# Optimization experiments

Measured on AMD Instinct MI355X. Metric: run time of the kernel, lower is better.

## Reference

```python
import jax, jax.numpy as jnp
import numpy as np

TAU = 0.02        # System2Reasoner softmax temperature
TOP_K = 50        # retrieval top-k
ALPHA = 1.0       # visual/text prototype mixing
TAU_CONF = 0.8    # entropy confidence threshold


def _normalize(x):
    return x / jnp.maximum(jnp.linalg.norm(x, axis=-1, keepdims=True), 1e-12)


def _entropy(logits):
    p = jax.nn.softmax(logits, axis=-1)
    return -jnp.sum(p * jnp.log(p + 1e-10))


def setup_inputs() -> dict:
    key = jax.random.key(0)
    k1, k2, k3, k4, k5, k6 = jax.random.split(key, 6)
    D, P, M, C = 768, 2048, 65536, 1000
    test_global = _normalize(jax.random.normal(k1, (1, D), dtype=jnp.float32))
    test_patches = _normalize(jax.random.normal(k2, (P, D), dtype=jnp.float32))
    memory_nodes = _normalize(jax.random.normal(k3, (M, D), dtype=jnp.float32))
    textual_anchors = _normalize(jax.random.normal(k4, (C, D), dtype=jnp.float32))
    class_sums = jax.random.normal(k5, (C, D), dtype=jnp.float32)
    class_counts = jax.random.uniform(k6, (C,), dtype=jnp.float32) * 100.0 + 1.0
    return {
        "test_global": test_global,
        "test_patches": test_patches,
        "memory_nodes": memory_nodes,
        "textual_anchors": textual_anchors,
        "class_sums": class_sums,
        "class_counts": class_counts,
        "max_steps": 3,
    }


def reference(test_global, test_patches, memory_nodes, textual_anchors,
              class_sums, class_counts, max_steps):
    # System-1 prototypes
    safe_counts = jnp.maximum(class_counts, 1.0)[:, None]            # [C,1]
    visual_protos = _normalize(class_sums / safe_counts)             # [C,D]
    protos = _normalize(textual_anchors + ALPHA * visual_protos)     # [C,D]

    sys1_logits = 100.0 * test_global @ protos.T                     # [1,C]
    active0 = _entropy(sys1_logits) > TAU_CONF

    def body(carry, _):
        patches, logits, step, active = carry
        # message passing: topk cosine-sim retrieval + softmax-weighted gather
        sim = patches @ memory_nodes.T                               # [P,M]
        topv, topi = jax.lax.top_k(sim, TOP_K)                       # [P,K]
        attn = jax.nn.softmax(topv / TAU, axis=1)                    # [P,K]
        gathered = memory_nodes[topi]                                # [P,K,D]
        messages = jnp.einsum('pk,pkd->pd', attn, gathered)          # [P,D]
        new_patches = _normalize(patches + messages)
        # token evidence pooling
        ev = jnp.max(new_patches @ textual_anchors.T, axis=-1, keepdims=True)  # [P,1]
        w = jax.nn.softmax(ev / TAU, axis=0)                         # [P,1]
        g = _normalize(jnp.sum(new_patches * w, axis=0, keepdims=True))        # [1,D]
        new_logits = 100.0 * g @ protos.T                            # [1,C]
        # only commit updates while the entropy loop is still active
        patches = jnp.where(active, new_patches, patches)
        logits = jnp.where(active, new_logits, logits)
        step = step + active.astype(jnp.int32)
        active = jnp.logical_and(active, _entropy(new_logits) > TAU_CONF)
        return (patches, logits, step, active), None

    (patches, final_logits, step, _), _ = jax.lax.scan(
        body, (test_patches, sys1_logits, jnp.int32(0), active0),
        None, length=max_steps)
    return final_logits, step
```

## Files before the change

### kernel.cpp

```cpp
#include <hip/hip_runtime.h>
#include <hip/hip_bf16.h>
#include <stdint.h>


typedef __attribute__((ext_vector_type(8))) short short8;
typedef __attribute__((ext_vector_type(4))) float f32x4;
typedef __attribute__((ext_vector_type(4))) int   i32x4;

#define DIM    768
#define NPATCH 2048
#define NMEM   65536
#define NCLS   1000
#define NSAMP  4096
#define CAP    1024
#define PRESEL 64
#define PCAP   128
#define TAUINV 50.0f

__device__ __forceinline__ unsigned short f2bf(float f){
  unsigned b = __float_as_uint(f);
  b += 0x7FFFu + ((b >> 16) & 1u);
  return (unsigned short)(b >> 16);
}
__device__ __forceinline__ unsigned encf(float x){
  unsigned b = __float_as_uint(x);
  return (b & 0x80000000u) ? ~b : (b | 0x80000000u);
}
__device__ __forceinline__ float decf(unsigned k){
  unsigned b = (k & 0x80000000u) ? (k & 0x7FFFFFFFu) : ~k;
  return __uint_as_float(b);
}
__device__ __forceinline__ void gload16(const void* g, void* l){
  __builtin_amdgcn_global_load_lds(
      (const __attribute__((address_space(1))) unsigned int*)g,
      (__attribute__((address_space(3))) unsigned int*)l, 16, 0, 0);
}
__device__ __forceinline__ uint4 pack8(float4 a, float4 b){
  uint4 u;
  u.x = (unsigned)f2bf(a.x) | ((unsigned)f2bf(a.y) << 16);
  u.y = (unsigned)f2bf(a.z) | ((unsigned)f2bf(a.w) << 16);
  u.z = (unsigned)f2bf(b.x) | ((unsigned)f2bf(b.y) << 16);
  u.w = (unsigned)f2bf(b.z) | ((unsigned)f2bf(b.w) << 16);
  return u;
}
__device__ __forceinline__ uint4 packq16(const float* s, float inv){
  unsigned wd[4];
  #pragma unroll
  for (int k = 0; k < 4; ++k){
    unsigned v = 0;
    #pragma unroll
    for (int j = 0; j < 4; ++j){
      int q = __float2int_rn(s[k*4 + j] * inv);
      q = q > 127 ? 127 : (q < -127 ? -127 : q);
      v |= ((unsigned)(q & 255)) << (8*j);
    }
    wd[k] = v;
  }
  return make_uint4(wd[0], wd[1], wd[2], wd[3]);
}

__device__ __forceinline__ unsigned select_kth(const unsigned* keys, int n, int k,
                                               unsigned* hist, int t)
{
  __syncthreads();
  if (t == 0){ hist[256] = 0u; hist[257] = (unsigned)k; }
  __syncthreads();
  for (int pass = 0; pass < 4; ++pass){
    int shift = 24 - 8*pass;
    hist[t] = 0u;
    __syncthreads();
    unsigned pref = hist[256];
    for (int i = t; i < n; i += 256){
      unsigned key = keys[i];
      bool ok = (pass == 0) || ((key >> (shift + 8)) == pref);
      if (ok) atomicAdd(&hist[(key >> shift) & 255u], 1u);
    }
    __syncthreads();
    if (t == 0){
      unsigned krem = hist[257];
      unsigned cum = 0u; int b = 255;
      for (; b >= 0; --b){ cum += hist[b]; if (cum >= krem) break; }
      if (b < 0) b = 0;
      unsigned above = cum - hist[b];
      hist[257] = krem - above;
      hist[256] = (pref << 8) | (unsigned)b;
    }
    __syncthreads();
  }
  return hist[256];
}

__global__ __launch_bounds__(256) void proto_kernel(
    const float* __restrict__ anchors, const float* __restrict__ sums,
    const float* __restrict__ counts, float* __restrict__ protos,
    unsigned short* __restrict__ anchors_bf)
{
  int c = blockIdx.x, t = threadIdx.x;
  if (c >= NCLS){
    for (int j = 0; j < 3; ++j) anchors_bf[(size_t)c*DIM + t + j*256] = 0;
    return;
  }
  __shared__ float wv[4]; __shared__ float bc;
  float cnt = fmaxf(counts[c], 1.0f);
  float v[3];
  #pragma unroll
  for (int j = 0; j < 3; ++j) v[j] = sums[(size_t)c*DIM + t + j*256] / cnt;
  float ss = v[0]*v[0] + v[1]*v[1] + v[2]*v[2];
  for (int off = 32; off > 0; off >>= 1) ss += __shfl_down(ss, off, 64);
  if ((t & 63) == 0) wv[t >> 6] = ss;
  __syncthreads();
  if (t == 0) bc = wv[0] + wv[1] + wv[2] + wv[3];
  __syncthreads();
  float rn = 1.0f / fmaxf(sqrtf(bc), 1e-12f);
  __syncthreads();
  float pr[3];
  #pragma unroll
  for (int j = 0; j < 3; ++j){
    int d = t + j*256;
    float a = anchors[(size_t)c*DIM + d];
    pr[j] = a + v[j] * rn;
    int dd = (d & ~63) | ((((d >> 3) ^ c) & 7) << 3) | (d & 7);
    anchors_bf[(size_t)c*DIM + dd] = f2bf(a);
  }
  ss = pr[0]*pr[0] + pr[1]*pr[1] + pr[2]*pr[2];
  for (int off = 32; off > 0; off >>= 1) ss += __shfl_down(ss, off, 64);
  if ((t & 63) == 0) wv[t >> 6] = ss;
  __syncthreads();
  if (t == 0) bc = wv[0] + wv[1] + wv[2] + wv[3];
  __syncthreads();
  float rn2 = 1.0f / fmaxf(sqrtf(bc), 1e-12f);
  #pragma unroll
  for (int j = 0; j < 3; ++j) protos[(size_t)c*DIM + t + j*256] = pr[j] * rn2;
}

__global__ __launch_bounds__(256) void prep_patches(
    const float* __restrict__ tp, float* __restrict__ pc)
{
  size_t i = (size_t)blockIdx.x*256 + threadIdx.x;
  *(float4*)(pc + i*4) = *(const float4*)(tp + i*4);
}

__global__ __launch_bounds__(512) void conv_i8_kernel(
    const float* __restrict__ src, signed char* __restrict__ dst,
    float* __restrict__ scales)
{
  int w = threadIdx.x >> 6, lane = threadIdx.x & 63;
  int row = blockIdx.x*8 + w;
  const float* r = src + (size_t)row*DIM;
  float x[16]; float mx = 0.f;
  if (lane < 48){
    #pragma unroll
    for (int j = 0; j < 4; ++j){
      float4 v = *(const float4*)(r + lane*16 + j*4);
      x[j*4+0] = v.x; x[j*4+1] = v.y; x[j*4+2] = v.z; x[j*4+3] = v.w;
      mx = fmaxf(mx, fmaxf(fmaxf(fabsf(v.x), fabsf(v.y)), fmaxf(fabsf(v.z), fabsf(v.w))));
    }
  }
  for (int off = 32; off > 0; off >>= 1) mx = fmaxf(mx, __shfl_xor(mx, off, 64));
  if (lane == 0) scales[row] = mx / 127.0f;
  float inv = (mx > 0.f) ? 127.0f / mx : 0.f;
  if (lane < 48){
    int ks = lane >> 2, c = lane & 3;
    uint4 u = packq16(x, inv);
    *(uint4*)(dst + (size_t)row*DIM + ks*64 + ((c ^ ((row >> 1) & 3))*16)) = u;
  }
}

__global__ __launch_bounds__(256) void slab_init(
    const float* __restrict__ pc, unsigned short* __restrict__ slab,
    signed char* __restrict__ sli8, float* __restrict__ spb)
{
  __shared__ __align__(16) float gl[DIM];
  __shared__ float wv[4]; __shared__ float bc;
  int p = blockIdx.x, t = threadIdx.x;
  float a0 = pc[(size_t)p*DIM + t], a1 = pc[(size_t)p*DIM + t + 256],
        a2 = pc[(size_t)p*DIM + t + 512];
  gl[t] = a0; gl[t + 256] = a1; gl[t + 512] = a2;
  float am = fmaxf(fabsf(a0), fmaxf(fabsf(a1), fabsf(a2)));
  for (int off = 32; off > 0; off >>= 1) am = fmaxf(am, __shfl_down(am, off, 64));
  if ((t & 63) == 0) wv[t >> 6] = am;
  __syncthreads();
  if (t == 0) bc = fmaxf(fmaxf(wv[0], wv[1]), fmaxf(wv[2], wv[3]));
  __syncthreads();
  float mx = bc;
  float inv8 = (mx > 0.f) ? 127.0f / mx : 0.f;
  if (t < 96){
    int ks2 = t >> 3, c8 = t & 7;
    const float* sblk = &gl[ks2*64 + c8*8];
    uint4 u = pack8(*(const float4*)sblk, *(const float4*)(sblk + 4));
    *(uint4*)((char*)slab + (((size_t)ks2*NPATCH + p)*128) + ((size_t)(c8 ^ (p & 7))*16)) = u;
  }
  if (t < 48){
    int ks2 = t >> 2, c = t & 3;
    uint4 u = packq16(&gl[t*16], inv8);
    *(uint4*)(sli8 + ((size_t)ks2*NPATCH + p)*64 + ((c ^ ((p >> 1) & 3))*16)) = u;
  }
  if (t == 0) spb[p] = mx / 127.0f;
}

template<int MODE, int NT>
__global__ __launch_bounds__(256, 3) void gemm8_kernel(
    const signed char* __restrict__ Ai8, const float* __restrict__ sA, int rowbase,
    const signed char* __restrict__ Bslab, const float* __restrict__ sB,
    const float* __restrict__ thresholds,
    int* __restrict__ counters,
    int* __restrict__ cand_idx,
    float* __restrict__ cand_score,
    float* __restrict__ sims_sample,
    const int* __restrict__ active)
{
  if (*active == 0) return;
  __shared__ __align__(16) signed char Al[128*64];
  __shared__ __align__(16) signed char Bl[128*64];
  int b = blockIdx.x, nwg = gridDim.x;
  int wg = (b & 7)*(nwg >> 3) + (b >> 3);
  int mt0 = (wg >> 4) * NT, pt = wg & 15;
  int t = threadIdx.x, w = t >> 6, lane = t & 63, l15 = lane & 15, l4 = lane >> 4;
  int wr = w >> 1, wc = w & 1;
  int pbase = pt*128;

  float thv[4], sbv[4];
  #pragma unroll
  for (int g = 0; g < 4; ++g){
    int patch = pbase + wc*64 + g*16 + l15;
    if (MODE == 0) thv[g] = thresholds[patch];
    sbv[g] = sB[patch];
  }

  i32x4 acc[4][4];
  #pragma unroll
  for (int x = 0; x < 4; ++x)
    #pragma unroll
    for (int y = 0; y < 4; ++y) acc[x][y] = (i32x4){0, 0, 0, 0};

  const int NSTEP = NT * 12;
  for (int s = 0; s < NSTEP; ++s){
    int tile = s / 12, ks = s % 12;
    if (s) __syncthreads();
    size_t arow0 = (size_t)rowbase + ((size_t)(mt0 + tile))*128;
    #pragma unroll
    for (int i = 0; i < 2; ++i){
      int g = w*64 + i*256 + lane;
      const void* ga = Ai8 + (arow0 + (g >> 2))*(size_t)DIM + ks*64 + (g & 3)*16;
      gload16(ga, (char*)Al + (w*64 + i*256)*16);
      const void* gb = Bslab + ((size_t)ks*NPATCH + pbase)*64 + (size_t)g*16;
      gload16(gb, (char*)Bl + (w*64 + i*256)*16);
    }
    __syncthreads();

    i32x4 af[4], bfr[4];
    #pragma unroll
    for (int ng = 0; ng < 4; ++ng){
      int row = wr*64 + ng*16 + l15;
      af[ng] = *(const i32x4*)(Al + row*64 + ((l4 ^ ((row >> 1) & 3))*16));
    }
    #pragma unroll
    for (int g = 0; g < 4; ++g){
      int row = wc*64 + g*16 + l15;
      bfr[g] = *(const i32x4*)(Bl + row*64 + ((l4 ^ ((row >> 1) & 3))*16));
    }
    #pragma unroll
    for (int ng = 0; ng < 4; ++ng)
      #pragma unroll
      for (int g = 0; g < 4; ++g)
        acc[ng][g] = __builtin_amdgcn_mfma_i32_16x16x64_i8(af[ng], bfr[g], acc[ng][g], 0, 0, 0);

    if (ks == 11){
      int nodebase = rowbase + (mt0 + tile)*128 + wr*64;
      if (MODE == 0){
        #pragma unroll
        for (int g = 0; g < 4; ++g){
          int patch = pbase + wc*64 + g*16 + l15;
          float th = thv[g], sb = sbv[g];
          #pragma unroll
          for (int ng = 0; ng < 4; ++ng){
            f32x4 sa = *(const f32x4*)(sA + nodebase + ng*16 + l4*4);
            #pragma unroll
            for (int i = 0; i < 4; ++i){
              float v = (float)acc[ng][g][i] * sa[i] * sb;
              if (v >= th){
                int node = nodebase + ng*16 + l4*4 + i;
                int pos = atomicAdd(&counters[patch], 1);
                if (pos < CAP){
                  cand_idx[(size_t)patch*CAP + pos]   = node;
                  cand_score[(size_t)patch*CAP + pos] = v;
                }
              }
            }
          }
        }
      } else {
        #pragma unroll
        for (int g = 0; g < 4; ++g){
          int patch = pbase + wc*64 + g*16 + l15;
          float sb = sbv[g];
          #pragma unroll
          for (int ng = 0; ng < 4; ++ng){
            f32x4 sa = *(const f32x4*)(sA + nodebase + ng*16 + l4*4);
            f32x4 v;
            #pragma unroll
            for (int i = 0; i < 4; ++i) v[i] = (float)acc[ng][g][i] * sa[i] * sb;
            int col = nodebase + ng*16 + l4*4;
            *(f32x4*)(sims_sample + (size_t)patch*NSAMP + col) = v;
          }
        }
      }
      if (tile + 1 < NT){
        #pragma unroll
        for (int x = 0; x < 4; ++x)
          #pragma unroll
          for (int y = 0; y < 4; ++y) acc[x][y] = (i32x4){0, 0, 0, 0};
      }
    }
  }
}

__global__ __launch_bounds__(256, 3) void gemm_ev_kernel(
    const unsigned short* __restrict__ Abf,
    const unsigned short* __restrict__ Bslab,
    unsigned* __restrict__ ev_key,
    const int* __restrict__ active)
{
  if (*active == 0) return;
  __shared__ __align__(16) unsigned short Al[128*64];
  __shared__ __align__(16) unsigned short Bl[128*64];
  int b = blockIdx.x, nwg = gridDim.x;
  int wg = (b & 7)*(nwg >> 3) + (b >> 3);
  int mt = wg >> 4, pt = wg & 15;
  int t = threadIdx.x, w = t >> 6, lane = t & 63, l15 = lane & 15, l4 = lane >> 4;
  int wr = w >> 1, wc = w & 1;
  int pbase = pt*128;
  int srow = w*8 + (lane >> 3);
  int scol = (lane & 7)*16;
  const char* Ab = (const char*)Abf;
  const char* Bb = (const char*)Bslab;

  f32x4 acc[4][4];
  #pragma unroll
  for (int x = 0; x < 4; ++x)
    #pragma unroll
    for (int y = 0; y < 4; ++y) acc[x][y] = (f32x4){0.f, 0.f, 0.f, 0.f};

  for (int s = 0; s < 12; ++s){
    if (s) __syncthreads();
    size_t arow0 = (size_t)mt*128;
    #pragma unroll
    for (int i = 0; i < 4; ++i){
      const void* ga = Ab + ((arow0 + srow + i*32)*(size_t)(DIM*2)) + s*128 + scol;
      gload16(ga, (char*)Al + i*4096 + w*1024);
      const void* gb = Bb + (((size_t)s*NPATCH + pbase)*128) + i*4096 + w*1024 + lane*16;
      gload16(gb, (char*)Bl + i*4096 + w*1024);
    }
    __syncthreads();
    short8 af[2][4], bf_[2][4];
    #pragma unroll
    for (int kk = 0; kk < 2; ++kk){
      #pragma unroll
      for (int ng = 0; ng < 4; ++ng){
        int row = wr*64 + ng*16 + l15;
        int slot = (kk*4 + l4) ^ (row & 7);
        af[kk][ng] = *(const short8*)((const char*)Al + row*128 + slot*16);
      }
      #pragma unroll
      for (int g = 0; g < 4; ++g){
        int row = wc*64 + g*16 + l15;
        int slot = (kk*4 + l4) ^ (row & 7);
        bf_[kk][g] = *(const short8*)((const char*)Bl + row*128 + slot*16);
      }
    }
    #pragma unroll
    for (int kk = 0; kk < 2; ++kk)
      #pragma unroll
      for (int ng = 0; ng < 4; ++ng)
        #pragma unroll
        for (int g = 0; g < 4; ++g)
          acc[ng][g] = __builtin_amdgcn_mfma_f32_16x16x32_bf16(af[kk][ng], bf_[kk][g], acc[ng][g], 0, 0, 0);
  }

  #pragma unroll
  for (int g = 0; g < 4; ++g){
    int patch = pbase + wc*64 + g*16 + l15;
    float m = -3e38f; bool any = false;
    #pragma unroll
    for (int ng = 0; ng < 4; ++ng){
      #pragma unroll
      for (int i = 0; i < 4; ++i){
        int a = mt*128 + wr*64 + ng*16 + l4*4 + i;
        if (a < NCLS){ m = fmaxf(m, acc[ng][g][i]); any = true; }
      }
    }
    if (any) atomicMax(&ev_key[patch], encf(m));
  }
}

__global__ __launch_bounds__(256) void thresh_kernel(
    const float* __restrict__ sims, float* __restrict__ thresholds,
    int* __restrict__ counters, int* __restrict__ cand_idx,
    float* __restrict__ cand_score, unsigned* __restrict__ ev_key,
    const int* __restrict__ active)
{
  if (*active == 0) return;
  __shared__ unsigned keys[NSAMP];
  __shared__ unsigned hist[258];
  __shared__ int lcnt;
  int p = blockIdx.x, t = threadIdx.x;
  const float4* src = (const float4*)(sims + (size_t)p*NSAMP);
  for (int i = t; i < NSAMP/4; i += 256){
    float4 v = src[i];
    keys[i*4+0] = encf(v.x); keys[i*4+1] = encf(v.y);
    keys[i*4+2] = encf(v.z); keys[i*4+3] = encf(v.w);
  }
  unsigned kth = select_kth(keys, NSAMP, 16, hist, t);
  if (t == 0){ thresholds[p] = decf(kth); ev_key[p] = 0u; lcnt = 0; }
  __syncthreads();
  for (int i = t; i < NSAMP; i += 256){
    unsigned key = keys[i];
    if (key >= kth){
      int pos = atomicAdd(&lcnt, 1);
      if (pos < CAP){
        cand_idx[(size_t)p*CAP + pos]   = i;
        cand_score[(size_t)p*CAP + pos] = decf(key);
      }
    }
  }
  __syncthreads();
  if (t == 0) counters[p] = lcnt < CAP ? lcnt : CAP;
}

__global__ __launch_bounds__(256) void msg_kernel(
    const int* __restrict__ counters, const int* __restrict__ cand_idx,
    const float* __restrict__ cand_score, const float* __restrict__ memf,
    float* __restrict__ pc, unsigned short* __restrict__ slab,
    signed char* __restrict__ sli8, float* __restrict__ spb,
    const int* __restrict__ active)
{
  if (*active == 0) return;
  __shared__ unsigned sk[CAP]; __shared__ int si[CAP];
  __shared__ __align__(16) float gl[DIM];
  __shared__ unsigned hist[258];
  __shared__ int pn[PCAP]; __shared__ float pv[PCAP];
  __shared__ float selv[64]; __shared__ int seli[64]; __shared__ float attn[64];
  __shared__ float wv[4]; __shared__ float bc;
  __shared__ int cnt2;
  int p = blockIdx.x, t = threadIdx.x;
  int n = counters[p]; if (n > CAP) n = CAP;
  #pragma unroll
  for (int j = 0; j < 3; ++j) gl[t + j*256] = pc[(size_t)p*DIM + t + j*256];
  for (int i = t; i < CAP; i += 256){
    sk[i] = (i < n) ? encf(cand_score[(size_t)p*CAP + i]) : 0u;
    si[i] = (i < n) ? cand_idx[(size_t)p*CAP + i] : 0;
  }
  unsigned kth64 = 1u;
  if (n > PRESEL) kth64 = select_kth(sk, n, PRESEL, hist, t);
  else            __syncthreads();
  if (t == 0) cnt2 = 0;
  __syncthreads();
  for (int i = t; i < n; i += 256){
    if (sk[i] >= kth64){
      int pos = atomicAdd(&cnt2, 1);
      if (pos < PCAP) pn[pos] = si[i];
    }
  }
  __syncthreads();
  int m = cnt2 < PCAP ? cnt2 : PCAP;
  int w = t >> 6, lane = t & 63;
  for (int i = w; i < m; i += 4){
    const float* row = memf + (size_t)pn[i]*DIM;
    float s = 0.f;
    #pragma unroll
    for (int j = 0; j < 12; ++j){
      int d = lane + j*64;
      s += row[d] * gl[d];
    }
    for (int off = 32; off > 0; off >>= 1) s += __shfl_down(s, off, 64);
    if (lane == 0) pv[i] = s;
  }
  __syncthreads();
  int K = m < 50 ? m : 50;
  if (t < m) sk[t] = encf(pv[t]);
  unsigned kth50 = 1u;
  if (m > K) kth50 = select_kth(sk, m, K, hist, t);
  else       __syncthreads();
  if (t == 0) cnt2 = 0;
  __syncthreads();
  if (t < m && sk[t] > kth50){
    int pos = atomicAdd(&cnt2, 1);
    seli[pos] = pn[t]; selv[pos] = pv[t];
    sk[t] = 0u;
  }
  __syncthreads();
  if (t == 0){
    int c = cnt2;
    for (int j = c; j < K; ++j){
      int best = -1, bestnode = 0x7FFFFFFF;
      for (int i = 0; i < m; ++i)
        if (sk[i] == kth50 && pn[i] < bestnode){ best = i; bestnode = pn[i]; }
      if (best < 0) break;
      seli[j] = pn[best]; selv[j] = pv[best]; sk[best] = 0u;
    }
  }
  __syncthreads();
  float v = (t < K) ? selv[t] : -3e38f;
  for (int off = 32; off > 0; off >>= 1) v = fmaxf(v, __shfl_down(v, off, 64));
  if ((t & 63) == 0) wv[t >> 6] = v;
  __syncthreads();
  if (t == 0) bc = fmaxf(fmaxf(wv[0], wv[1]), fmaxf(wv[2], wv[3]));
  __syncthreads();
  float vmax = bc;
  __syncthreads();
  if (t < K) attn[t] = __expf((selv[t] - vmax) * TAUINV);
  __syncthreads();
  if (t == 0){ float s = 0.f; for (int k = 0; k < K; ++k) s += attn[k]; bc = s; }
  __syncthreads();
  float inv = 1.0f / bc;
  int d0 = t, d1 = t + 256, d2 = t + 512;
  float a0 = gl[d0], a1 = gl[d1], a2 = gl[d2];
  for (int k = 0; k < K; ++k){
    float a = attn[k] * inv;
    const float* row = memf + (size_t)seli[k]*DIM;
    a0 += a * row[d0]; a1 += a * row[d1]; a2 += a * row[d2];
  }
  float ss = a0*a0 + a1*a1 + a2*a2;
  for (int off = 32; off > 0; off >>= 1) ss += __shfl_down(ss, off, 64);
  if ((t & 63) == 0) wv[t >> 6] = ss;
  __syncthreads();
  if (t == 0) bc = wv[0] + wv[1] + wv[2] + wv[3];
  __syncthreads();
  float rn = 1.0f / fmaxf(sqrtf(bc), 1e-12f);
  a0 *= rn; a1 *= rn; a2 *= rn;
  float* orow = pc + (size_t)p*DIM;
  orow[d0] = a0; orow[d1] = a1; orow[d2] = a2;
  float am = fmaxf(fabsf(a0), fmaxf(fabsf(a1), fabsf(a2)));
  for (int off = 32; off > 0; off >>= 1) am = fmaxf(am, __shfl_down(am, off, 64));
  __syncthreads();
  gl[d0] = a0; gl[d1] = a1; gl[d2] = a2;
  if ((t & 63) == 0) wv[t >> 6] = am;
  __syncthreads();
  if (t == 0) bc = fmaxf(fmaxf(wv[0], wv[1]), fmaxf(wv[2], wv[3]));
  __syncthreads();
  float mx = bc;
  float inv8 = (mx > 0.f) ? 127.0f / mx : 0.f;
  if (t < 96){
    int ks2 = t >> 3, c8 = t & 7;
    const float* sblk = &gl[ks2*64 + c8*8];
    uint4 u = pack8(*(const float4*)sblk, *(const float4*)(sblk + 4));
    *(uint4*)((char*)slab + (((size_t)ks2*NPATCH + p)*128) + ((size_t)(c8 ^ (p & 7))*16)) = u;
  }
  if (t < 48){
    int ks2 = t >> 2, c = t & 3;
    uint4 u = packq16(&gl[t*16], inv8);
    *(uint4*)(sli8 + ((size_t)ks2*NPATCH + p)*64 + ((c ^ ((p >> 1) & 3))*16)) = u;
  }
  if (t == 0) spb[p] = mx / 127.0f;
}

__global__ __launch_bounds__(256) void pl2_kernel(
    const unsigned* __restrict__ ev_key, const float* __restrict__ pc,
    float* __restrict__ g_part, const int* __restrict__ active)
{
  if (*active == 0) return;
  __shared__ float wv[4]; __shared__ float bc;
  int t = threadIdx.x;
  float m = -3e38f;
  for (int i = t; i < NPATCH; i += 256) m = fmaxf(m, decf(ev_key[i]));
  for (int off = 32; off > 0; off >>= 1) m = fmaxf(m, __shfl_down(m, off, 64));
  if ((t & 63) == 0) wv[t >> 6] = m;
  __syncthreads();
  if (t == 0) bc = fmaxf(fmaxf(wv[0], wv[1]), fmaxf(wv[2], wv[3]));
  __syncthreads();
  float M = bc;
  __syncthreads();
  float s = 0.f;
  for (int i = t; i < NPATCH; i += 256) s += __expf((decf(ev_key[i]) - M) * TAUINV);
  for (int off = 32; off > 0; off >>= 1) s += __shfl_down(s, off, 64);
  if ((t & 63) == 0) wv[t >> 6] = s;
  __syncthreads();
  if (t == 0) bc = wv[0] + wv[1] + wv[2] + wv[3];
  __syncthreads();
  float invS = 1.0f / bc;
  int pbase = blockIdx.x * 64;
  float a0 = 0.f, a1 = 0.f, a2 = 0.f;
  for (int i = 0; i < 64; ++i){
    int p = pbase + i;
    float wgt = __expf((decf(ev_key[p]) - M) * TAUINV) * invS;
    const float* row = pc + (size_t)p*DIM;
    a0 += wgt * row[t]; a1 += wgt * row[t + 256]; a2 += wgt * row[t + 512];
  }
  g_part[blockIdx.x*DIM + t]       = a0;
  g_part[blockIdx.x*DIM + t + 256] = a1;
  g_part[blockIdx.x*DIM + t + 512] = a2;
}

template<bool INIT>
__global__ __launch_bounds__(256) void cm_kernel(
    const float* __restrict__ gsrc, const float* __restrict__ protos,
    float* __restrict__ logits_cur, int* __restrict__ step, int* __restrict__ active)
{
  if (!INIT && *active == 0) return;
  __shared__ __align__(16) float gl[DIM];
  __shared__ float lg[NCLS];
  __shared__ float wv[4]; __shared__ float bc;
  int t = threadIdx.x;
  if (INIT){
    #pragma unroll
    for (int j = 0; j < 3; ++j) gl[t + j*256] = gsrc[t + j*256];
  } else {
    float gv[3]; float ss = 0.f;
    #pragma unroll
    for (int j = 0; j < 3; ++j){
      int d = t + j*256;
      float s = 0.f;
      for (int b2 = 0; b2 < 32; ++b2) s += gsrc[b2*DIM + d];
      gv[j] = s; ss += s*s;
    }
    for (int off = 32; off > 0; off >>= 1) ss += __shfl_down(ss, off, 64);
    if ((t & 63) == 0) wv[t >> 6] = ss;
    __syncthreads();
    if (t == 0) bc = wv[0] + wv[1] + wv[2] + wv[3];
    __syncthreads();
    float rn = 1.0f / fmaxf(sqrtf(bc), 1e-12f);
    #pragma unroll
    for (int j = 0; j < 3; ++j) gl[t + j*256] = gv[j] * rn;
  }
  __syncthreads();
  for (int c = t; c < NCLS; c += 256){
    const float4* pr = (const float4*)(protos + (size_t)c*DIM);
    float s = 0.f;
    #pragma unroll 4
    for (int d4 = 0; d4 < DIM/4; ++d4){
      float4 pv = pr[d4];
      float4 gv = *(const float4*)&gl[d4*4];
      s += gv.x*pv.x + gv.y*pv.y + gv.z*pv.z + gv.w*pv.w;
    }
    float L = 100.0f * s;
    lg[c] = L; logits_cur[c] = L;
  }
  __syncthreads();
  float m = -3e38f;
  for (int c = t; c < NCLS; c += 256) m = fmaxf(m, lg[c]);
  for (int off = 32; off > 0; off >>= 1) m = fmaxf(m, __shfl_down(m, off, 64));
  if ((t & 63) == 0) wv[t >> 6] = m;
  __syncthreads();
  if (t == 0) bc = fmaxf(fmaxf(wv[0], wv[1]), fmaxf(wv[2], wv[3]));
  __syncthreads();
  float M = bc;
  __syncthreads();
  float s = 0.f;
  for (int c = t; c < NCLS; c += 256) s += __expf(lg[c] - M);
  for (int off = 32; off > 0; off >>= 1) s += __shfl_down(s, off, 64);
  if ((t & 63) == 0) wv[t >> 6] = s;
  __syncthreads();
  if (t == 0) bc = wv[0] + wv[1] + wv[2] + wv[3];
  __syncthreads();
  float S = bc;
  __syncthreads();
  float hp = 0.f;
  for (int c = t; c < NCLS; c += 256){
    float pcl = __expf(lg[c] - M) / S;
    hp += pcl * __logf(pcl + 1e-10f);
  }
  for (int off = 32; off > 0; off >>= 1) hp += __shfl_down(hp, off, 64);
  if ((t & 63) == 0) wv[t >> 6] = hp;
  __syncthreads();
  if (t == 0){
    float H = -(wv[0] + wv[1] + wv[2] + wv[3]);
    if (INIT){ *step = 0; *active = (H > 0.8f) ? 1 : 0; }
    else     { *step = *step + 1; *active = (H > 0.8f) ? 1 : 0; }
  }
}

__global__ void pub_kernel(const float* __restrict__ logits_cur, const int* __restrict__ step,
                           float* __restrict__ out)
{
  int i = blockIdx.x*256 + threadIdx.x;
  if (i < NCLS) out[i] = logits_cur[i];
  else if (i == NCLS) out[i] = (float)(*step);
}

extern "C" void kernel_launch(void* const* d_in, const int* in_sizes, int n_in,
                              void* d_out, int out_size, void* d_ws, size_t ws_size,
                              hipStream_t stream)
{
  (void)in_sizes; (void)n_in; (void)out_size; (void)ws_size;
  const float* tg  = (const float*)d_in[0];
  const float* tp  = (const float*)d_in[1];
  const float* mem = (const float*)d_in[2];
  const float* anc = (const float*)d_in[3];
  const float* cs  = (const float*)d_in[4];
  const float* cc  = (const float*)d_in[5];

  char* ws = (char*)d_ws;
  auto al = [](size_t x){ return (x + 255) & ~(size_t)255; };
  size_t OFF_PC   = 0;
  size_t OFF_PROT = al(OFF_PC   + (size_t)NPATCH*DIM*4);
  size_t OFF_ABF  = al(OFF_PROT + (size_t)NCLS*DIM*4);
  size_t OFF_MI8  = al(OFF_ABF  + (size_t)1024*DIM*2);
  size_t OFF_SA   = al(OFF_MI8  + (size_t)NMEM*DIM);
  size_t OFF_SLAB = al(OFF_SA   + (size_t)NMEM*4);
  size_t OFF_SLI8 = al(OFF_SLAB + (size_t)NPATCH*DIM*2);
  size_t OFF_SPB  = al(OFF_SLI8 + (size_t)NPATCH*DIM);
  size_t OFF_SS   = al(OFF_SPB  + (size_t)NPATCH*4);
  size_t OFF_THR  = al(OFF_SS   + (size_t)NPATCH*NSAMP*4);
  size_t OFF_CNT  = al(OFF_THR  + (size_t)NPATCH*4);
  size_t OFF_CI   = al(OFF_CNT  + (size_t)NPATCH*4);
  size_t OFF_CSC  = al(OFF_CI   + (size_t)NPATCH*CAP*4);
  size_t OFF_EV   = al(OFF_CSC  + (size_t)NPATCH*CAP*4);
  size_t OFF_GP   = al(OFF_EV   + (size_t)NPATCH*4);
  size_t OFF_LC   = al(OFF_GP   + (size_t)32*DIM*4);
  size_t OFF_STEP = al(OFF_LC   + (size_t)NCLS*4);

  float*          pc      = (float*)(ws + OFF_PC);
  float*          protos  = (float*)(ws + OFF_PROT);
  unsigned short* abf     = (unsigned short*)(ws + OFF_ABF);
  signed char*    mi8     = (signed char*)(ws + OFF_MI8);
  float*          sa      = (float*)(ws + OFF_SA);
  unsigned short* slab    = (unsigned short*)(ws + OFF_SLAB);
  signed char*    sli8    = (signed char*)(ws + OFF_SLI8);
  float*          spb     = (float*)(ws + OFF_SPB);
  float*          simss   = (float*)(ws + OFF_SS);
  float*          thr     = (float*)(ws + OFF_THR);
  int*            cnt     = (int*)(ws + OFF_CNT);
  int*            ci      = (int*)(ws + OFF_CI);
  float*          csc     = (float*)(ws + OFF_CSC);
  unsigned*       evk     = (unsigned*)(ws + OFF_EV);
  float*          gp      = (float*)(ws + OFF_GP);
  float*          lc      = (float*)(ws + OFF_LC);
  int*            stepp   = (int*)(ws + OFF_STEP);
  int*            activep = stepp + 1;

  proto_kernel<<<1024, 256, 0, stream>>>(anc, cs, cc, protos, abf);
  prep_patches<<<(NPATCH*DIM/4)/256, 256, 0, stream>>>(tp, pc);
  conv_i8_kernel<<<NMEM/8, 512, 0, stream>>>(mem, mi8, sa);
  cm_kernel<true><<<1, 256, 0, stream>>>(tg, protos, lc, stepp, activep);
  slab_init<<<NPATCH, 256, 0, stream>>>(pc, slab, sli8, spb);

  for (int it = 0; it < 3; ++it){
    gemm8_kernel<1,1><<<(NSAMP/128)*16, 256, 0, stream>>>(
        mi8, sa, 0, sli8, spb, thr, cnt, ci, csc, simss, activep);
    thresh_kernel<<<NPATCH, 256, 0, stream>>>(simss, thr, cnt, ci, csc, evk, activep);
    gemm8_kernel<0,4><<<((NMEM-NSAMP)/512)*16, 256, 0, stream>>>(
        mi8, sa, NSAMP, sli8, spb, thr, cnt, ci, csc, simss, activep);
    msg_kernel<<<NPATCH, 256, 0, stream>>>(cnt, ci, csc, mem, pc, slab, sli8, spb, activep);
    gemm_ev_kernel<<<(1024/128)*16, 256, 0, stream>>>(abf, slab, evk, activep);
    pl2_kernel<<<32, 256, 0, stream>>>(evk, pc, gp, activep);
    cm_kernel<false><<<1, 256, 0, stream>>>(gp, protos, lc, stepp, activep);
  }
  pub_kernel<<<4, 256, 0, stream>>>(lc, stepp, (float*)d_out);
}
```

Before: 1.739 ms.

## Double-buffer LDS tiles in int8 similarity GEMM and enlarge per-block tile count

```diff
diff --git a/kernel.cpp b/kernel.cpp
--- a/kernel.cpp
+++ b/kernel.cpp
@@ -210,8 +210,8 @@
     const int* __restrict__ active)
 {
   if (*active == 0) return;
-  __shared__ __align__(16) signed char Al[128*64];
-  __shared__ __align__(16) signed char Bl[128*64];
+  __shared__ __align__(16) signed char Al[2][128*64];
+  __shared__ __align__(16) signed char Bl[2][128*64];
   int b = blockIdx.x, nwg = gridDim.x;
   int wg = (b & 7)*(nwg >> 3) + (b >> 3);
   int mt0 = (wg >> 4) * NT, pt = wg & 15;
@@ -227,37 +227,43 @@
     sbv[g] = sB[patch];
   }
 
-  i32x4 acc[4][4];
-  #pragma unroll
-  for (int x = 0; x < 4; ++x)
-    #pragma unroll
-    for (int y = 0; y < 4; ++y) acc[x][y] = (i32x4){0, 0, 0, 0};
-
-  const int NSTEP = NT * 12;
-  for (int s = 0; s < NSTEP; ++s){
+  auto STAGE = [&](int s, int bsel){
     int tile = s / 12, ks = s % 12;
-    if (s) __syncthreads();
     size_t arow0 = (size_t)rowbase + ((size_t)(mt0 + tile))*128;
     #pragma unroll
     for (int i = 0; i < 2; ++i){
       int g = w*64 + i*256 + lane;
       const void* ga = Ai8 + (arow0 + (g >> 2))*(size_t)DIM + ks*64 + (g & 3)*16;
-      gload16(ga, (char*)Al + (w*64 + i*256)*16);
+      gload16(ga, (char*)Al[bsel] + (w*64 + i*256)*16);
       const void* gb = Bslab + ((size_t)ks*NPATCH + pbase)*64 + (size_t)g*16;
-      gload16(gb, (char*)Bl + (w*64 + i*256)*16);
-    }
-    __syncthreads();
+      gload16(gb, (char*)Bl[bsel] + (w*64 + i*256)*16);
+    }
+  };
+
+  i32x4 acc[4][4];
+  #pragma unroll
+  for (int x = 0; x < 4; ++x)
+    #pragma unroll
+    for (int y = 0; y < 4; ++y) acc[x][y] = (i32x4){0, 0, 0, 0};
+
+  const int NSTEP = NT * 12;
+  STAGE(0, 0);
+  __syncthreads();
+
+  for (int s = 0; s < NSTEP; ++s){
+    int cur = s & 1;
+    if (s + 1 < NSTEP) STAGE(s + 1, cur ^ 1);
 
     i32x4 af[4], bfr[4];
     #pragma unroll
     for (int ng = 0; ng < 4; ++ng){
       int row = wr*64 + ng*16 + l15;
-      af[ng] = *(const i32x4*)(Al + row*64 + ((l4 ^ ((row >> 1) & 3))*16));
+      af[ng] = *(const i32x4*)(Al[cur] + row*64 + ((l4 ^ ((row >> 1) & 3))*16));
     }
     #pragma unroll
     for (int g = 0; g < 4; ++g){
       int row = wc*64 + g*16 + l15;
-      bfr[g] = *(const i32x4*)(Bl + row*64 + ((l4 ^ ((row >> 1) & 3))*16));
+      bfr[g] = *(const i32x4*)(Bl[cur] + row*64 + ((l4 ^ ((row >> 1) & 3))*16));
     }
     #pragma unroll
     for (int ng = 0; ng < 4; ++ng)
@@ -265,7 +271,8 @@
       for (int g = 0; g < 4; ++g)
         acc[ng][g] = __builtin_amdgcn_mfma_i32_16x16x64_i8(af[ng], bfr[g], acc[ng][g], 0, 0, 0);
 
-    if (ks == 11){
+    if ((s % 12) == 11){
+      int tile = s / 12;
       int nodebase = rowbase + (mt0 + tile)*128 + wr*64;
       if (MODE == 0){
         #pragma unroll
@@ -305,13 +312,14 @@
           }
         }
       }
-      if (tile + 1 < NT){
+      if (s + 1 < NSTEP){
         #pragma unroll
         for (int x = 0; x < 4; ++x)
           #pragma unroll
           for (int y = 0; y < 4; ++y) acc[x][y] = (i32x4){0, 0, 0, 0};
       }
     }
+    __syncthreads();
   }
 }
 
@@ -446,9 +454,9 @@
   int n = counters[p]; if (n > CAP) n = CAP;
   #pragma unroll
   for (int j = 0; j < 3; ++j) gl[t + j*256] = pc[(size_t)p*DIM + t + j*256];
-  for (int i = t; i < CAP; i += 256){
-    sk[i] = (i < n) ? encf(cand_score[(size_t)p*CAP + i]) : 0u;
-    si[i] = (i < n) ? cand_idx[(size_t)p*CAP + i] : 0;
+  for (int i = t; i < n; i += 256){
+    sk[i] = encf(cand_score[(size_t)p*CAP + i]);
+    si[i] = cand_idx[(size_t)p*CAP + i];
   }
   unsigned kth64 = 1u;
   if (n > PRESEL) kth64 = select_kth(sk, n, PRESEL, hist, t);
@@ -738,7 +746,7 @@
     gemm8_kernel<1,1><<<(NSAMP/128)*16, 256, 0, stream>>>(
         mi8, sa, 0, sli8, spb, thr, cnt, ci, csc, simss, activep);
     thresh_kernel<<<NPATCH, 256, 0, stream>>>(simss, thr, cnt, ci, csc, evk, activep);
-    gemm8_kernel<0,4><<<((NMEM-NSAMP)/512)*16, 256, 0, stream>>>(
+    gemm8_kernel<0,5><<<((NMEM-NSAMP)/640)*16, 256, 0, stream>>>(
         mi8, sa, NSAMP, sli8, spb, thr, cnt, ci, csc, simss, activep);
     msg_kernel<<<NPATCH, 256, 0, stream>>>(cnt, ci, csc, mem, pc, slab, sli8, spb, activep);
     gemm_ev_kernel<<<(1024/128)*16, 256, 0, stream>>>(abf, slab, evk, activep);
```

After: 1.810 ms. 1.04x slower.
